# Kernel tuning notes

Measured on AMD Instinct MI355X. Metric: run time of the kernel, lower is better.

Reference implementation:

```python
import jax, jax.numpy as jnp
import numpy as np

B, N, E, H = 2, 2048, 256, 4
DK = E // H


def setup_inputs() -> dict:
    key = jax.random.key(0)
    ks = jax.random.split(key, 7)
    xav = lambda k, shape, fan_in, fan_out: jax.random.uniform(
        k, shape, minval=-1.0, maxval=1.0, dtype=jnp.float32
    ) * np.sqrt(6.0 / (fan_in + fan_out))
    return {
        "node_embeddings": jax.random.normal(ks[0], (B, N, E), dtype=jnp.float32),
        "adjacency_matrices": jax.random.randint(ks[1], (B, N, N), 0, 2, dtype=jnp.int32),
        "Wq": xav(ks[2], (H, E, DK), E, DK),
        "Wk": xav(ks[3], (H, E, DK), E, DK),
        "Wv": xav(ks[4], (H, E, DK), E, DK),
        "Wo": xav(ks[5], (E, E), E, E),
        "bo": jnp.zeros((E,), dtype=jnp.float32),
    }


def reference(node_embeddings, adjacency_matrices, Wq, Wk, Wv, Wo, bo):
    # Per-head projections: (B,N,E) x (H,E,dk) -> (B,H,N,dk)
    Q = jnp.einsum("bnd,hde->bhne", node_embeddings, Wq)
    K = jnp.einsum("bnd,hde->bhne", node_embeddings, Wk)
    V = jnp.einsum("bnd,hde->bhne", node_embeddings, Wv)
    scale = 1.0 / np.sqrt(DK).astype(np.float32)
    # (B,H,N,N) scores, adjacency-masked
    scores = jnp.einsum("bhne,bhme->bhnm", Q, K) * scale
    mask = adjacency_matrices[:, None, :, :] > 0  # (B,1,N,N) -> broadcast over H
    scores = jnp.where(mask, scores, -jnp.inf)
    attn = jax.nn.softmax(scores, axis=-1)
    heads = jnp.einsum("bhnm,bhme->bhne", attn, V)  # (B,H,N,dk)
    concat = heads.transpose(0, 2, 1, 3).reshape(node_embeddings.shape[0], node_embeddings.shape[1], E)
    return concat @ Wo.T + bo
```

## Files before the change

kernel.cpp:

```cpp
#include <hip/hip_runtime.h>
#include <hip/hip_bf16.h>
#include <math.h>

#define Bb 2
#define Nn 2048
#define Ee 256
#define Hh 4
#define DKk 64

typedef __bf16 bf16x8 __attribute__((ext_vector_type(8)));
typedef float f32x4 __attribute__((ext_vector_type(4)));

#define QSCALE 0.18033688011112042f
#define MOFF 20.0f

__global__ void __launch_bounds__(256) pack_adj(const int* __restrict__ adj,
                                                unsigned long long* __restrict__ bits) {
    int t = threadIdx.x;
    int wid = t >> 6, lane = t & 63;
    #pragma unroll
    for (int i = 0; i < 4; ++i) {
        int gid = blockIdx.x * 16 + i * 4 + wid;
        int row = gid >> 3;
        int g = gid & 7;
        const int4* src = (const int4*)(adj + (size_t)row * Nn + g * 256) + lane;
        int4 v = *src;
        unsigned long long b0 = __ballot(v.x > 0);
        unsigned long long b1 = __ballot(v.y > 0);
        unsigned long long b2 = __ballot(v.z > 0);
        unsigned long long b3 = __ballot(v.w > 0);
        if (lane == 0) {
            ulonglong2* dst = (ulonglong2*)(bits + (size_t)gid * 4);
            ulonglong2 p0; p0.x = b0; p0.y = b1;
            ulonglong2 p1; p1.x = b2; p1.y = b3;
            dst[0] = p0;
            dst[1] = p1;
        }
    }
}

__global__ void __launch_bounds__(256) pack_all(
        const float* __restrict__ x,
        const float* __restrict__ Wq,
        const float* __restrict__ Wk,
        const float* __restrict__ Wv,
        const float* __restrict__ Wo,
        __bf16* __restrict__ xb,
        __bf16* __restrict__ WB,
        __bf16* __restrict__ WoB) {
    int blk = blockIdx.x, t = threadIdx.x;
    if (blk < 1024) {
        size_t i = ((size_t)blk * 256 + t) * 4;
        float4 v = *(const float4*)(x + i);
        __bf16 o[4] = {(__bf16)v.x, (__bf16)v.y, (__bf16)v.z, (__bf16)v.w};
        *(ushort4*)(xb + i) = *(ushort4*)o;
    } else if (blk < 1024 + 768) {
        int row = blk - 1024;
        int m = row >> 8, h = (row >> 6) & 3, e = row & 63;
        const float* W = (m == 0 ? Wq : (m == 1 ? Wk : Wv));
        float sc = (m == 0) ? QSCALE : 1.0f;
        WB[(size_t)row * 256 + t] = (__bf16)(W[h * 16384 + t * 64 + e] * sc);
    } else {
        int blk2 = blk - 1792;
        size_t i = ((size_t)blk2 * 256 + t) * 4;
        float4 v = *(const float4*)(Wo + i);
        __bf16 o[4] = {(__bf16)v.x, (__bf16)v.y, (__bf16)v.z, (__bf16)v.w};
        *(ushort4*)(WoB + i) = *(ushort4*)o;
    }
}

__global__ void __launch_bounds__(256) qkv_mfma(
        const __bf16* __restrict__ xb,
        const __bf16* __restrict__ WB,
        __bf16* __restrict__ Qb,
        __bf16* __restrict__ Kf,
        __bf16* __restrict__ Vf) {
    int bm = blockIdx.x;
    int t = threadIdx.x;
    int wid = t >> 6, lane = t & 63, li = lane & 15, quad = lane >> 4;
    int row0 = bm * 16;

    bf16x8 a[8];
    const __bf16* ap = xb + (size_t)(row0 + li) * 256 + quad * 8;
    #pragma unroll
    for (int i = 0; i < 8; ++i) a[i] = *(const bf16x8*)(ap + i * 32);

    int b = row0 >> 11;
    int nloc = row0 & 2047;

    #pragma unroll 1
    for (int j = 0; j < 12; ++j) {
        int c0 = wid * 192 + j * 16;
        const __bf16* bp = WB + (size_t)(c0 + li) * 256 + quad * 8;
        f32x4 acc = (f32x4){0.f, 0.f, 0.f, 0.f};
        #pragma unroll
        for (int i = 0; i < 8; ++i) {
            bf16x8 bfrag = *(const bf16x8*)(bp + i * 32);
            acc = __builtin_amdgcn_mfma_f32_16x16x32_bf16(a[i], bfrag, acc, 0, 0, 0);
        }
        int m = c0 >> 8;
        int h = (c0 >> 6) & 3;
        int e0 = c0 & 63;
        int bh = b * 4 + h;
        if (m == 0) {
            size_t base = ((size_t)bh * Nn + nloc + quad * 4) * 64 + e0 + li;
            #pragma unroll
            for (int r = 0; r < 4; ++r) Qb[base + (size_t)r * 64] = (__bf16)acc[r];
        } else if (m == 1) {
            int e = e0 + li;
            int cp = e >> 5, ek = e & 31;
            int qA = ek >> 3, jA = ek & 7;
            int kt = nloc >> 4;
            size_t ub = (((size_t)(bh * 128 + kt)) * 2 + cp) * 512 + qA * 128 + jA;
            #pragma unroll
            for (int r = 0; r < 4; ++r) Kf[ub + (quad * 4 + r) * 8] = (__bf16)acc[r];
        } else {
            int e = e0 + li;
            int et = e >> 4, liA = e & 15;
            int key32 = nloc >> 5;
            int nnb = nloc & 16;
            size_t ub = (((size_t)(bh * 64 + key32)) * 4 + et) * 512 + liA * 8;
            #pragma unroll
            for (int r = 0; r < 4; ++r) {
                int nn = nnb + quad * 4 + r;
                Vf[ub + (nn >> 3) * 128 + (nn & 7)] = (__bf16)acc[r];
            }
        }
    }
}

__global__ void __launch_bounds__(256, 3) attn_kernel(
        const __bf16* __restrict__ Qb,
        const __bf16* __restrict__ Kf,
        const __bf16* __restrict__ Vf,
        const unsigned long long* __restrict__ bits,
        __bf16* __restrict__ heads) {
    __shared__ __align__(16) __bf16 PS[4][16][72];
    __shared__ float OL[4][16][68];
    __shared__ float lL[4][16];

    int blk = blockIdx.x;
    int bh = blk >> 7, qt = blk & 127;
    int b = bh >> 2, h = bh & 3;
    int t = threadIdx.x;
    int wid = t >> 6, lane = t & 63, li = lane & 15, quad = lane >> 4;
    int q0 = qt * 16;

    const __bf16* qp = Qb + ((size_t)bh * Nn + q0 + li) * 64 + quad * 8;
    bf16x8 qa0 = *(const bf16x8*)qp;
    bf16x8 qa1 = *(const bf16x8*)(qp + 32);

    f32x4 o[4];
    #pragma unroll
    for (int et = 0; et < 4; ++et) o[et] = (f32x4){0.f, 0.f, 0.f, 0.f};
    f32x4 ls = (f32x4){0.f, 0.f, 0.f, 0.f};

    const __bf16* Kfb = Kf + (size_t)bh * 131072;
    const __bf16* Vfb = Vf + (size_t)bh * 131072;
    int lanew = lane * 8;

    #pragma unroll 1
    for (int g = 0; g < 2; ++g) {
        int grp = wid * 2 + g;
        unsigned long long aw[4];
        #pragma unroll
        for (int r = 0; r < 4; ++r)
            aw[r] = bits[(((size_t)b * Nn + q0 + quad * 4 + r) * 8 + grp) * 4 + (li & 3)];

        #pragma unroll 1
        for (int tt = 0; tt < 4; ++tt) {
            int key64 = grp * 4 + tt;

            bf16x8 kb[4][2];
            #pragma unroll
            for (int nt = 0; nt < 4; ++nt)
                #pragma unroll
                for (int c = 0; c < 2; ++c)
                    kb[nt][c] = *(const bf16x8*)(Kfb + ((size_t)((key64 * 4 + nt) * 2 + c)) * 512 + lanew);
            bf16x8 vb[4][2];
            #pragma unroll
            for (int et = 0; et < 4; ++et)
                #pragma unroll
                for (int kc = 0; kc < 2; ++kc)
                    vb[et][kc] = *(const bf16x8*)(Vfb + ((size_t)((key64 * 2 + kc) * 4 + et)) * 512 + lanew);

            f32x4 s[4];
            #pragma unroll
            for (int nt = 0; nt < 4; ++nt) {
                f32x4 z = (f32x4){-MOFF, -MOFF, -MOFF, -MOFF};
                z = __builtin_amdgcn_mfma_f32_16x16x32_bf16(qa0, kb[nt][0], z, 0, 0, 0);
                s[nt] = __builtin_amdgcn_mfma_f32_16x16x32_bf16(qa1, kb[nt][1], z, 0, 0, 0);
            }

            int shb = tt * 16 + (li >> 2);
            #pragma unroll
            for (int nt = 0; nt < 4; ++nt) {
                #pragma unroll
                for (int r = 0; r < 4; ++r) {
                    unsigned bit = (unsigned)(aw[r] >> (shb + nt * 4)) & 1u;
                    float p = bit ? __builtin_amdgcn_exp2f(s[nt][r]) : 0.f;
                    ls[r] += p;
                    PS[wid][quad * 4 + r][nt * 16 + li] = (__bf16)p;
                }
            }

            bf16x8 pa0 = *(const bf16x8*)&PS[wid][li][quad * 8];
            bf16x8 pa1 = *(const bf16x8*)&PS[wid][li][quad * 8 + 32];

            #pragma unroll
            for (int et = 0; et < 4; ++et) {
                o[et] = __builtin_amdgcn_mfma_f32_16x16x32_bf16(pa0, vb[et][0], o[et], 0, 0, 0);
                o[et] = __builtin_amdgcn_mfma_f32_16x16x32_bf16(pa1, vb[et][1], o[et], 0, 0, 0);
            }
        }
    }

    #pragma unroll
    for (int r = 0; r < 4; ++r) {
        float v = ls[r];
        v += __shfl_xor(v, 1, 64);
        v += __shfl_xor(v, 2, 64);
        v += __shfl_xor(v, 4, 64);
        v += __shfl_xor(v, 8, 64);
        if (li == 0) lL[wid][quad * 4 + r] = v;
        #pragma unroll
        for (int et = 0; et < 4; ++et)
            OL[wid][quad * 4 + r][et * 16 + li] = o[et][r];
    }
    __syncthreads();

    int qi = t >> 4, e0 = (t & 15) * 4;
    float l = lL[0][qi] + lL[1][qi] + lL[2][qi] + lL[3][qi];
    float inv = 1.0f / l;
    float s0 = 0.f, s1 = 0.f, s2 = 0.f, s3 = 0.f;
    #pragma unroll
    for (int w = 0; w < 4; ++w) {
        s0 += OL[w][qi][e0];
        s1 += OL[w][qi][e0 + 1];
        s2 += OL[w][qi][e0 + 2];
        s3 += OL[w][qi][e0 + 3];
    }
    __bf16 ob[4] = {(__bf16)(s0 * inv), (__bf16)(s1 * inv),
                    (__bf16)(s2 * inv), (__bf16)(s3 * inv)};
    __bf16* dst = heads + ((size_t)b * Nn + q0 + qi) * 256 + h * 64 + e0;
    *(ushort4*)dst = *(ushort4*)ob;
}

__global__ void __launch_bounds__(256) outproj_mfma(
        const __bf16* __restrict__ hb,
        const __bf16* __restrict__ WoB,
        const float* __restrict__ bo,
        float* __restrict__ out) {
    int bm = blockIdx.x;
    int t = threadIdx.x;
    int wid = t >> 6, lane = t & 63, li = lane & 15, quad = lane >> 4;
    int row0 = bm * 16;

    bf16x8 a[8];
    const __bf16* ap = hb + (size_t)(row0 + li) * 256 + quad * 8;
    #pragma unroll
    for (int i = 0; i < 8; ++i) a[i] = *(const bf16x8*)(ap + i * 32);

    #pragma unroll 1
    for (int j = 0; j < 4; ++j) {
        int c0 = wid * 64 + j * 16;
        const __bf16* bp = WoB + (size_t)(c0 + li) * 256 + quad * 8;
        f32x4 acc = (f32x4){0.f, 0.f, 0.f, 0.f};
        #pragma unroll
        for (int i = 0; i < 8; ++i) {
            bf16x8 bfrag = *(const bf16x8*)(bp + i * 32);
            acc = __builtin_amdgcn_mfma_f32_16x16x32_bf16(a[i], bfrag, acc, 0, 0, 0);
        }
        int c = c0 + li;
        float bias = bo[c];
        size_t base = ((size_t)row0 + quad * 4) * 256 + c;
        #pragma unroll
        for (int r = 0; r < 4; ++r) out[base + (size_t)r * 256] = acc[r] + bias;
    }
}

extern "C" void kernel_launch(void* const* d_in, const int* in_sizes, int n_in,
                              void* d_out, int out_size, void* d_ws, size_t ws_size,
                              hipStream_t stream) {
    const float* x   = (const float*)d_in[0];
    const int*   adj = (const int*)d_in[1];
    const float* Wq  = (const float*)d_in[2];
    const float* Wk  = (const float*)d_in[3];
    const float* Wv  = (const float*)d_in[4];
    const float* Wo  = (const float*)d_in[5];
    const float* bo  = (const float*)d_in[6];
    float* out = (float*)d_out;

    char* ws = (char*)d_ws;
    const size_t MB = 1024 * 1024;
    __bf16* Qb  = (__bf16*)(ws);
    __bf16* Kf  = (__bf16*)(ws + 2 * MB);
    __bf16* Vf  = (__bf16*)(ws + 4 * MB);
    unsigned long long* bits = (unsigned long long*)(ws + 6 * MB);
    __bf16* xb  = (__bf16*)(ws + 7 * MB);
    __bf16* WB  = (__bf16*)(ws + 9 * MB);
    __bf16* WoB = (__bf16*)(ws + 9 * MB + 512 * 1024);
    __bf16* headsb = xb;

    pack_adj<<<2048, 256, 0, stream>>>(adj, bits);
    pack_all<<<1856, 256, 0, stream>>>(x, Wq, Wk, Wv, Wo, xb, WB, WoB);
    qkv_mfma<<<256, 256, 0, stream>>>(xb, WB, Qb, Kf, Vf);
    attn_kernel<<<Bb * Hh * (Nn / 16), 256, 0, stream>>>(Qb, Kf, Vf, bits, headsb);
    outproj_mfma<<<256, 256, 0, stream>>>(headsb, WoB, bo, out);
}
```

Measured before the change: 137.2 us.

## Merge pack kernels, convert x to bf16 inside QKV kernel, raise attn occupancy

```diff
diff --git a/kernel.cpp b/kernel.cpp
--- a/kernel.cpp
+++ b/kernel.cpp
@@ -14,54 +14,45 @@
 #define QSCALE 0.18033688011112042f
 #define MOFF 20.0f
 
-__global__ void __launch_bounds__(256) pack_adj(const int* __restrict__ adj,
-                                                unsigned long long* __restrict__ bits) {
-    int t = threadIdx.x;
-    int wid = t >> 6, lane = t & 63;
-    #pragma unroll
-    for (int i = 0; i < 4; ++i) {
-        int gid = blockIdx.x * 16 + i * 4 + wid;
-        int row = gid >> 3;
-        int g = gid & 7;
-        const int4* src = (const int4*)(adj + (size_t)row * Nn + g * 256) + lane;
-        int4 v = *src;
-        unsigned long long b0 = __ballot(v.x > 0);
-        unsigned long long b1 = __ballot(v.y > 0);
-        unsigned long long b2 = __ballot(v.z > 0);
-        unsigned long long b3 = __ballot(v.w > 0);
-        if (lane == 0) {
-            ulonglong2* dst = (ulonglong2*)(bits + (size_t)gid * 4);
-            ulonglong2 p0; p0.x = b0; p0.y = b1;
-            ulonglong2 p1; p1.x = b2; p1.y = b3;
-            dst[0] = p0;
-            dst[1] = p1;
-        }
-    }
-}
-
-__global__ void __launch_bounds__(256) pack_all(
-        const float* __restrict__ x,
+__global__ void __launch_bounds__(256) pack_kernel(
+        const int* __restrict__ adj,
         const float* __restrict__ Wq,
         const float* __restrict__ Wk,
         const float* __restrict__ Wv,
         const float* __restrict__ Wo,
-        __bf16* __restrict__ xb,
+        unsigned long long* __restrict__ bits,
         __bf16* __restrict__ WB,
         __bf16* __restrict__ WoB) {
     int blk = blockIdx.x, t = threadIdx.x;
-    if (blk < 1024) {
-        size_t i = ((size_t)blk * 256 + t) * 4;
-        float4 v = *(const float4*)(x + i);
-        __bf16 o[4] = {(__bf16)v.x, (__bf16)v.y, (__bf16)v.z, (__bf16)v.w};
-        *(ushort4*)(xb + i) = *(ushort4*)o;
-    } else if (blk < 1024 + 768) {
-        int row = blk - 1024;
+    if (blk < 2048) {
+        int wid = t >> 6, lane = t & 63;
+        #pragma unroll
+        for (int i = 0; i < 4; ++i) {
+            int gid = blk * 16 + i * 4 + wid;
+            int row = gid >> 3;
+            int g = gid & 7;
+            const int4* src = (const int4*)(adj + (size_t)row * Nn + g * 256) + lane;
+            int4 v = *src;
+            unsigned long long b0 = __ballot(v.x > 0);
+            unsigned long long b1 = __ballot(v.y > 0);
+            unsigned long long b2 = __ballot(v.z > 0);
+            unsigned long long b3 = __ballot(v.w > 0);
+            if (lane == 0) {
+                ulonglong2* dst = (ulonglong2*)(bits + (size_t)gid * 4);
+                ulonglong2 p0; p0.x = b0; p0.y = b1;
+                ulonglong2 p1; p1.x = b2; p1.y = b3;
+                dst[0] = p0;
+                dst[1] = p1;
+            }
+        }
+    } else if (blk < 2816) {
+        int row = blk - 2048;
         int m = row >> 8, h = (row >> 6) & 3, e = row & 63;
         const float* W = (m == 0 ? Wq : (m == 1 ? Wk : Wv));
         float sc = (m == 0) ? QSCALE : 1.0f;
         WB[(size_t)row * 256 + t] = (__bf16)(W[h * 16384 + t * 64 + e] * sc);
     } else {
-        int blk2 = blk - 1792;
+        int blk2 = blk - 2816;
         size_t i = ((size_t)blk2 * 256 + t) * 4;
         float4 v = *(const float4*)(Wo + i);
         __bf16 o[4] = {(__bf16)v.x, (__bf16)v.y, (__bf16)v.z, (__bf16)v.w};
@@ -70,7 +61,7 @@
 }
 
 __global__ void __launch_bounds__(256) qkv_mfma(
-        const __bf16* __restrict__ xb,
+        const float* __restrict__ x,
         const __bf16* __restrict__ WB,
         __bf16* __restrict__ Qb,
         __bf16* __restrict__ Kf,
@@ -81,9 +72,15 @@
     int row0 = bm * 16;
 
     bf16x8 a[8];
-    const __bf16* ap = xb + (size_t)(row0 + li) * 256 + quad * 8;
-    #pragma unroll
-    for (int i = 0; i < 8; ++i) a[i] = *(const bf16x8*)(ap + i * 32);
+    const float* xp = x + (size_t)(row0 + li) * 256 + quad * 8;
+    #pragma unroll
+    for (int i = 0; i < 8; ++i) {
+        float4 f0 = *(const float4*)(xp + i * 32);
+        float4 f1 = *(const float4*)(xp + i * 32 + 4);
+        __bf16 tmp[8] = {(__bf16)f0.x, (__bf16)f0.y, (__bf16)f0.z, (__bf16)f0.w,
+                         (__bf16)f1.x, (__bf16)f1.y, (__bf16)f1.z, (__bf16)f1.w};
+        a[i] = *(bf16x8*)tmp;
+    }
 
     int b = row0 >> 11;
     int nloc = row0 & 2047;
@@ -129,7 +126,7 @@
     }
 }
 
-__global__ void __launch_bounds__(256, 3) attn_kernel(
+__global__ void __launch_bounds__(256, 4) attn_kernel(
         const __bf16* __restrict__ Qb,
         const __bf16* __restrict__ Kf,
         const __bf16* __restrict__ Vf,
@@ -144,6 +141,7 @@
     int b = bh >> 2, h = bh & 3;
     int t = threadIdx.x;
     int wid = t >> 6, lane = t & 63, li = lane & 15, quad = lane >> 4;
+    int li2 = li >> 2;
     int q0 = qt * 16;
 
     const __bf16* qp = Qb + ((size_t)bh * Nn + q0 + li) * 64 + quad * 8;
@@ -192,12 +190,14 @@
                 s[nt] = __builtin_amdgcn_mfma_f32_16x16x32_bf16(qa1, kb[nt][1], z, 0, 0, 0);
             }
 
-            int shb = tt * 16 + (li >> 2);
+            unsigned halfw[4];
+            #pragma unroll
+            for (int r = 0; r < 4; ++r) halfw[r] = (unsigned)(aw[r] >> (tt * 16));
             #pragma unroll
             for (int nt = 0; nt < 4; ++nt) {
                 #pragma unroll
                 for (int r = 0; r < 4; ++r) {
-                    unsigned bit = (unsigned)(aw[r] >> (shb + nt * 4)) & 1u;
+                    unsigned bit = (halfw[r] >> (li2 + nt * 4)) & 1u;
                     float p = bit ? __builtin_amdgcn_exp2f(s[nt][r]) : 0.f;
                     ls[r] += p;
                     PS[wid][quad * 4 + r][nt * 16 + li] = (__bf16)p;
@@ -297,14 +297,12 @@
     __bf16* Kf  = (__bf16*)(ws + 2 * MB);
     __bf16* Vf  = (__bf16*)(ws + 4 * MB);
     unsigned long long* bits = (unsigned long long*)(ws + 6 * MB);
-    __bf16* xb  = (__bf16*)(ws + 7 * MB);
-    __bf16* WB  = (__bf16*)(ws + 9 * MB);
-    __bf16* WoB = (__bf16*)(ws + 9 * MB + 512 * 1024);
-    __bf16* headsb = xb;
-
-    pack_adj<<<2048, 256, 0, stream>>>(adj, bits);
-    pack_all<<<1856, 256, 0, stream>>>(x, Wq, Wk, Wv, Wo, xb, WB, WoB);
-    qkv_mfma<<<256, 256, 0, stream>>>(xb, WB, Qb, Kf, Vf);
+    __bf16* WB  = (__bf16*)(ws + 7 * MB);
+    __bf16* WoB = (__bf16*)(ws + 7 * MB + 512 * 1024);
+    __bf16* headsb = (__bf16*)(ws + 8 * MB);
+
+    pack_kernel<<<2880, 256, 0, stream>>>(adj, Wq, Wk, Wv, Wo, bits, WB, WoB);
+    qkv_mfma<<<256, 256, 0, stream>>>(x, WB, Qb, Kf, Vf);
     attn_kernel<<<Bb * Hh * (Nn / 16), 256, 0, stream>>>(Qb, Kf, Vf, bits, headsb);
     outproj_mfma<<<256, 256, 0, stream>>>(headsb, WoB, bo, out);
 }
```

After: 143.9 us. 1.05x slower.
